# Optimization experiments

Hardware: AMD Instinct MI355X
Metric: run time of the kernel (lower is better)

The kernel has to match this reference:

```python
import jax, jax.numpy as jnp
import numpy as np

DIM = 512
NUM_HEADS = 8
DIM_HEAD = DIM // NUM_HEADS


def _xavier(key, shape):
    fan_in, fan_out = shape[0], shape[1]
    a = (6.0 / (fan_in + fan_out)) ** 0.5
    return jax.random.uniform(key, shape, jnp.float32, -a, a)


def setup_inputs() -> dict:
    key = jax.random.key(0)
    ks = jax.random.split(key, 8)
    B, N, M = 2, 2048, 2048
    x = jax.random.normal(ks[0], (B, N, DIM), jnp.float32)
    source = jax.random.normal(ks[1], (B, M, DIM), jnp.float32)
    source_mask = jax.random.randint(ks[2], (B, M), 0, 2) > 0
    Wq = _xavier(ks[3], (DIM, DIM)); bq = jnp.zeros((DIM,), jnp.float32)
    Wk = _xavier(ks[4], (DIM, DIM)); bk = jnp.zeros((DIM,), jnp.float32)
    Wv = _xavier(ks[5], (DIM, DIM)); bv = jnp.zeros((DIM,), jnp.float32)
    Wm = _xavier(ks[6], (DIM, DIM)); bm = jnp.zeros((DIM,), jnp.float32)
    return {"x": x, "source": source, "source_mask": source_mask,
            "Wq": Wq, "bq": bq, "Wk": Wk, "bk": bk,
            "Wv": Wv, "bv": bv, "Wm": Wm, "bm": bm}


def reference(x, source, source_mask, Wq, bq, Wk, bk, Wv, bv, Wm, bm):
    B, N, D = x.shape
    M = source.shape[-2]
    H, Dh = NUM_HEADS, DIM_HEAD
    # projections (torch Linear: x @ W^T + b)
    q = (x @ Wq.T + bq).reshape(B, N, H, Dh)
    k = (source @ Wk.T + bk).reshape(B, M, H, Dh)
    v = (source @ Wv.T + bv).reshape(B, M, H, Dh)
    scale = 1.0 / (Dh ** 0.5)
    # scores: [B, N, M, H]
    scores = jnp.einsum('bnhd,bmhd->bnmh', q, k) * scale
    scores = jnp.where(source_mask[:, None, :, None], scores, -jnp.inf)
    prob = jax.nn.softmax(scores, axis=-2)  # softmax over m
    agg = jnp.einsum('bnmh,bmhd->bnhd', prob, v).reshape(B, N, D)
    return agg @ Wm.T + bm
```

## Files before the change

### kernel.cpp

```cpp
#include <hip/hip_runtime.h>
#include <hip/hip_bf16.h>

#define DIMF 512
#define NHEAD 8
#define DHEAD 64
#define BATCH 2
#define SEQN 2048
#define SEQM 2048
#define FPS 40
#define QSCALE 0.18033688011112042f

typedef unsigned short u16;
typedef __attribute__((ext_vector_type(8))) short bf16x8;
typedef __attribute__((ext_vector_type(4))) float f32x4;

static __device__ __forceinline__ u16 f2bf(float f) {
    unsigned u = __float_as_uint(f);
    u += 0x7FFF + ((u >> 16) & 1);
    return (u16)(u >> 16);
}
static __device__ __forceinline__ u16 f2bf_fast(float f) {
    return (u16)((__float_as_uint(f) + 0x8000u) >> 16);
}

static __device__ __forceinline__
void load16(const u16* g, u16* l) {
    __builtin_amdgcn_global_load_lds(
        (const __attribute__((address_space(1))) void*)g,
        (__attribute__((address_space(3))) void*)l,
        16, 0, 0);
}

__global__ __launch_bounds__(256)
void cvt_w(const float* __restrict__ wq, const float* __restrict__ wk,
           const float* __restrict__ wv, const float* __restrict__ wm,
           const int* __restrict__ mask,
           u16* __restrict__ wqb, u16* __restrict__ wkb,
           u16* __restrict__ wvb, u16* __restrict__ wmb,
           u16* __restrict__ maskbf)
{
    int i = (blockIdx.x * 256 + threadIdx.x) * 4;
    if (blockIdx.y == 4) {
        if (i < BATCH * SEQM) {
            int4 m4 = *(const int4*)&mask[i];
            *(ushort4*)&maskbf[i] = make_ushort4(m4.x ? 0x3F80 : 0, m4.y ? 0x3F80 : 0,
                                                 m4.z ? 0x3F80 : 0, m4.w ? 0x3F80 : 0);
        }
        return;
    }
    const float* in = (blockIdx.y == 0) ? wq : (blockIdx.y == 1) ? wk
                    : (blockIdx.y == 2) ? wv : wm;
    u16* out = (blockIdx.y == 0) ? wqb : (blockIdx.y == 1) ? wkb
             : (blockIdx.y == 2) ? wvb : wmb;
    if (i >= DIMF * DIMF) return;
    float4 v = *(const float4*)&in[i];
    *(ushort4*)&out[i] = make_ushort4(f2bf(v.x), f2bf(v.y), f2bf(v.z), f2bf(v.w));
}

#define ASZ (64 * FPS)
#define BSZ (128 * FPS)

__device__ __forceinline__
void gemm_mfma(const float* __restrict__ Xf, const u16* __restrict__ Xb,
               const u16* __restrict__ W, const float* __restrict__ bias,
               const int* __restrict__ msk, void* __restrict__ Out, int mode)
{
    __shared__ __align__(16) u16 SH[2 * ASZ + 2 * BSZ];

    const int tid  = threadIdx.x;
    const int wave = tid >> 6;
    const int lane = tid & 63;
    const int l15  = lane & 15;
    const int quad = lane >> 4;
    const int wm = wave & 1, wn = wave >> 1;
    const int r0 = blockIdx.x * 64, c0 = blockIdx.y * 128;

    f32x4 acc[2][4] = {};

    const int br = tid >> 2, boct = tid & 3;
    const int ar = tid >> 3, aseg = tid & 7;

    bf16x8 rb0, rb1, rab;
    float4 ra0, ra1;

    auto loadg = [&](int k0) {
        rb0 = *(const bf16x8*)&W[(size_t)(c0 + br) * DIMF + k0 + boct * 8];
        rb1 = *(const bf16x8*)&W[(size_t)(c0 + br + 64) * DIMF + k0 + boct * 8];
        if (Xf) {
            ra0 = *(const float4*)&Xf[(size_t)(r0 + ar) * DIMF + k0 + aseg * 4];
            ra1 = *(const float4*)&Xf[(size_t)(r0 + ar + 32) * DIMF + k0 + aseg * 4];
        } else {
            rab = *(const bf16x8*)&Xb[(size_t)(r0 + br) * DIMF + k0 + boct * 8];
        }
    };
    auto stage = [&](int buf) {
        u16* As = SH + buf * ASZ;
        u16* Bs = SH + 2 * ASZ + buf * BSZ;
        if (Xf) {
            *(ushort4*)&As[ar * FPS + aseg * 4] =
                make_ushort4(f2bf(ra0.x), f2bf(ra0.y), f2bf(ra0.z), f2bf(ra0.w));
            *(ushort4*)&As[(ar + 32) * FPS + aseg * 4] =
                make_ushort4(f2bf(ra1.x), f2bf(ra1.y), f2bf(ra1.z), f2bf(ra1.w));
        } else {
            *(bf16x8*)&As[br * FPS + boct * 8] = rab;
        }
        *(bf16x8*)&Bs[br * FPS + boct * 8] = rb0;
        *(bf16x8*)&Bs[(br + 64) * FPS + boct * 8] = rb1;
    };

    loadg(0);
    stage(0);
    loadg(32);
    __syncthreads();

    const int NK = DIMF / 32;
    for (int kt = 0; kt < NK; ++kt) {
        const int cur = kt & 1;
        if (kt + 1 < NK) stage(cur ^ 1);
        if (kt + 2 < NK) loadg((kt + 2) * 32);
        const u16* As = SH + cur * ASZ;
        const u16* Bs = SH + 2 * ASZ + cur * BSZ;

        bf16x8 af[2], bf[4];
        #pragma unroll
        for (int mi = 0; mi < 2; ++mi)
            af[mi] = *(const bf16x8*)&As[(wm * 32 + mi * 16 + l15) * FPS + quad * 8];
        #pragma unroll
        for (int ni = 0; ni < 4; ++ni)
            bf[ni] = *(const bf16x8*)&Bs[(wn * 64 + ni * 16 + l15) * FPS + quad * 8];
        #pragma unroll
        for (int mi = 0; mi < 2; ++mi)
            #pragma unroll
            for (int ni = 0; ni < 4; ++ni)
                acc[mi][ni] = __builtin_amdgcn_mfma_f32_16x16x32_bf16(
                    af[mi], bf[ni], acc[mi][ni], 0, 0, 0);
        __syncthreads();
    }

    float bb[4];
    #pragma unroll
    for (int ni = 0; ni < 4; ++ni)
        bb[ni] = bias[c0 + wn * 64 + ni * 16 + l15];

    if (mode == 2) {
        u16* T = SH;
        const int b = r0 >> 11;
        const int n_base = r0 & (SEQN - 1);
        #pragma unroll
        for (int hh = 0; hh < 2; ++hh) {
            __syncthreads();
            if (wn == hh) {
                #pragma unroll
                for (int mi = 0; mi < 2; ++mi) {
                    const int rl = wm * 32 + mi * 16 + quad * 4;
                    int4 m4 = *(const int4*)&msk[b * SEQM + n_base + rl];
                    float mm[4];
                    mm[0] = m4.x ? 1.f : 0.f; mm[1] = m4.y ? 1.f : 0.f;
                    mm[2] = m4.z ? 1.f : 0.f; mm[3] = m4.w ? 1.f : 0.f;
                    #pragma unroll
                    for (int ni = 0; ni < 4; ++ni)
                        #pragma unroll
                        for (int r = 0; r < 4; ++r)
                            T[(rl + r) * 72 + ni * 16 + l15] =
                                f2bf((acc[mi][ni][r] + bb[ni]) * mm[r]);
                }
            }
            __syncthreads();
            const int d = tid >> 2, ms = (tid & 3) << 4;
            u16 tmp[16];
            #pragma unroll
            for (int j = 0; j < 16; ++j) tmp[j] = T[(ms + j) * 72 + d];
            const int hgl = (c0 >> 6) + hh;
            u16* dst = (u16*)Out + ((size_t)(b * NHEAD + hgl) * DHEAD + d) * SEQM
                       + n_base + ms;
            *(bf16x8*)&dst[0] = *(bf16x8*)&tmp[0];
            *(bf16x8*)&dst[8] = *(bf16x8*)&tmp[8];
        }
        return;
    }

    #pragma unroll
    for (int mi = 0; mi < 2; ++mi) {
        const int Rbase = r0 + wm * 32 + mi * 16 + quad * 4;
        const int b = Rbase >> 11;
        const int nb = Rbase & (SEQN - 1);
        #pragma unroll
        for (int ni = 0; ni < 4; ++ni) {
            const int C = c0 + wn * 64 + ni * 16 + l15;
            const int h = C >> 6, d = C & 63;
            if (mode == 0) {
                u16* ow = (u16*)Out;
                #pragma unroll
                for (int r = 0; r < 4; ++r)
                    ow[(((size_t)(b * NHEAD + h) * SEQN) + nb + r) * DHEAD + d] =
                        f2bf((acc[mi][ni][r] + bb[ni]) * QSCALE);
            } else if (mode == 1) {
                u16* ow = (u16*)Out;
                #pragma unroll
                for (int r = 0; r < 4; ++r)
                    ow[(((size_t)(b * NHEAD + h) * SEQN) + nb + r) * DHEAD + d] =
                        f2bf(acc[mi][ni][r] + bb[ni]);
            } else {
                float* ow = (float*)Out;
                #pragma unroll
                for (int r = 0; r < 4; ++r)
                    ow[(size_t)(Rbase + r) * DIMF + C] = acc[mi][ni][r] + bb[ni];
            }
        }
    }
}

__global__ __launch_bounds__(256, 3)
void qkv_proj(const float* __restrict__ x, const float* __restrict__ src,
              const u16* __restrict__ wqb, const float* __restrict__ bq,
              const u16* __restrict__ wkb, const float* __restrict__ bk,
              const u16* __restrict__ wvb, const float* __restrict__ bv,
              const int* __restrict__ mask,
              u16* __restrict__ qw, u16* __restrict__ kw, u16* __restrict__ vtw)
{
    const int z = blockIdx.z;
    const float* X = (z == 0) ? x : src;
    const u16* W = (z == 0) ? wqb : (z == 1) ? wkb : wvb;
    const float* B = (z == 0) ? bq : (z == 1) ? bk : bv;
    void* O = (z == 0) ? (void*)qw : (z == 1) ? (void*)kw : (void*)vtw;
    gemm_mfma(X, nullptr, W, B, mask, O, z);
}

__global__ __launch_bounds__(256, 3)
void out_proj(const u16* __restrict__ aggb, const u16* __restrict__ wmb,
              const float* __restrict__ bm, float* __restrict__ out)
{
    gemm_mfma(nullptr, aggb, wmb, bm, nullptr, (void*)out, 3);
}

__global__ __launch_bounds__(256, 2)
void flash_attn_mfma(const u16* __restrict__ q, const u16* __restrict__ k,
                     const u16* __restrict__ vt, const u16* __restrict__ maskbf,
                     u16* __restrict__ agg)
{
    __shared__ __align__(16) u16 KsD[2][4096];
    __shared__ __align__(16) u16 VtsD[2][4096];
    __shared__ u16 Ps[4 * 32 * FPS];
    float* Osum = (float*)&KsD[0][0];
    float* Lsum = (float*)&VtsD[0][0];

    const int tid  = threadIdx.x;
    const int wave = tid >> 6;
    const int lane = tid & 63;
    const int l15  = lane & 15;
    const int quad = lane >> 4;
    const int qg = wave >> 1, mh = wave & 1;

    const int bid  = blockIdx.x;
    const int xcd  = bid & 7, slot = bid >> 3;
    const int pair = (xcd << 1) | (slot & 1);
    const int b = pair >> 3, h = pair & 7;
    const int n0 = (slot >> 1) * 64;

    const size_t hoff = (size_t)(b * NHEAD + h) * (size_t)SEQM * DHEAD;
    const u16* kb = k  + hoff;
    const u16* vb = vt + hoff;
    const u16* mb = maskbf + b * SEQM;

    const int dr   = lane >> 3;
    const int doct = (lane & 7) ^ (dr & 7);
    const int g0 = wave, g1 = 4 + wave;
    const u16* kq0 = kb + (size_t)(g0 * 8 + dr) * DHEAD + doct * 8;
    const u16* kq1 = kb + (size_t)(g1 * 8 + dr) * DHEAD + doct * 8;
    const u16* vq0 = vb + (size_t)(g0 * 8 + dr) * SEQM + doct * 8;
    const u16* vq1 = vb + (size_t)(g1 * 8 + dr) * SEQM + doct * 8;

    bf16x8 qf[2][2];
    #pragma unroll
    for (int qh = 0; qh < 2; ++qh) {
        const u16* qp = q + hoff + (size_t)(n0 + qg * 32 + qh * 16 + l15) * DHEAD
                        + quad * 8;
        qf[qh][0] = *(const bf16x8*)qp;
        qf[qh][1] = *(const bf16x8*)(qp + 32);
    }

    load16(kq0, &KsD[0][g0 * 512]);
    load16(kq1, &KsD[0][g1 * 512]);
    load16(vq0, &VtsD[0][g0 * 512]);
    load16(vq1, &VtsD[0][g1 * 512]);
    bf16x8 mf_nxt = *(const bf16x8*)&mb[32 * mh + quad * 8];

    f32x4 O[2][4] = {};
    f32x4 lacc[2] = {};
    u16* Pw = Ps + wave * (32 * FPS);
    const int xoct = l15 & 7;

    for (int mt = 0; mt < SEQM / 64; ++mt) {
        const int cur = mt & 1;
        __syncthreads();
        bf16x8 mf = mf_nxt;
        if (mt + 1 < SEQM / 64) {
            const int m1 = (mt + 1) * 64;
            const int nb = cur ^ 1;
            load16(kq0 + (size_t)m1 * DHEAD, &KsD[nb][g0 * 512]);
            load16(kq1 + (size_t)m1 * DHEAD, &KsD[nb][g1 * 512]);
            load16(vq0 + m1, &VtsD[nb][g0 * 512]);
            load16(vq1 + m1, &VtsD[nb][g1 * 512]);
            mf_nxt = *(const bf16x8*)&mb[m1 + 32 * mh + quad * 8];
        }
        const u16* Ks  = KsD[cur];
        const u16* Vts = VtsD[cur];

        f32x4 st[2][2] = {};
        #pragma unroll
        for (int sub = 0; sub < 2; ++sub) {
            const int mrow = 32 * mh + 16 * sub + l15;
            #pragma unroll
            for (int c = 0; c < 2; ++c) {
                const int oct = (4 * c + quad) ^ xoct;
                bf16x8 af = *(const bf16x8*)&Ks[mrow * 64 + oct * 8];
                #pragma unroll
                for (int qh = 0; qh < 2; ++qh)
                    st[qh][sub] = __builtin_amdgcn_mfma_f32_16x16x32_bf16(
                        af, qf[qh][c], st[qh][sub], 0, 0, 0);
            }
        }

        #pragma unroll
        for (int qh = 0; qh < 2; ++qh)
            #pragma unroll
            for (int sub = 0; sub < 2; ++sub) {
                ushort4 w4 = make_ushort4(
                    f2bf_fast(__builtin_amdgcn_exp2f(st[qh][sub][0])),
                    f2bf_fast(__builtin_amdgcn_exp2f(st[qh][sub][1])),
                    f2bf_fast(__builtin_amdgcn_exp2f(st[qh][sub][2])),
                    f2bf_fast(__builtin_amdgcn_exp2f(st[qh][sub][3])));
                *(ushort4*)&Pw[(qh * 16 + l15) * FPS + 16 * sub + 4 * quad] = w4;
            }

        bf16x8 vf[4];
        #pragma unroll
        for (int sd = 0; sd < 4; ++sd) {
            const int oct = (4 * mh + quad) ^ xoct;
            vf[sd] = *(const bf16x8*)&Vts[(16 * sd + l15) * 64 + oct * 8];
        }

        #pragma unroll
        for (int qh = 0; qh < 2; ++qh) {
            bf16x8 pf = *(const bf16x8*)&Pw[(qh * 16 + l15) * FPS + quad * 8];
            lacc[qh] = __builtin_amdgcn_mfma_f32_16x16x32_bf16(pf, mf, lacc[qh], 0, 0, 0);
            #pragma unroll
            for (int sd = 0; sd < 4; ++sd)
                O[qh][sd] = __builtin_amdgcn_mfma_f32_16x16x32_bf16(
                    pf, vf[sd], O[qh][sd], 0, 0, 0);
        }
    }

    __syncthreads();
    if (mh == 1) {
        #pragma unroll
        for (int qh = 0; qh < 2; ++qh) {
            #pragma unroll
            for (int sd = 0; sd < 4; ++sd)
                #pragma unroll
                for (int r = 0; r < 4; ++r)
                    Osum[qg * 2048 + (qh * 16 + quad * 4 + r) * 64 + 16 * sd + l15]
                        = O[qh][sd][r];
            if (l15 == 0) {
                #pragma unroll
                for (int r = 0; r < 4; ++r)
                    Lsum[qg * 32 + qh * 16 + quad * 4 + r] = lacc[qh][r];
            }
        }
    }
    __syncthreads();
    if (mh == 0) {
        #pragma unroll
        for (int qh = 0; qh < 2; ++qh)
            #pragma unroll
            for (int r = 0; r < 4; ++r) {
                const float inv = 1.f /
                    (lacc[qh][r] + Lsum[qg * 32 + qh * 16 + quad * 4 + r]);
                const int n = n0 + qg * 32 + qh * 16 + quad * 4 + r;
                u16* ag = agg + ((size_t)b * SEQN + n) * DIMF + h * DHEAD + l15;
                #pragma unroll
                for (int sd = 0; sd < 4; ++sd)
                    ag[16 * sd] = f2bf((O[qh][sd][r] +
                        Osum[qg * 2048 + (qh * 16 + quad * 4 + r) * 64 + 16 * sd + l15])
                        * inv);
            }
    }
}

extern "C" void kernel_launch(void* const* d_in, const int* in_sizes, int n_in,
                              void* d_out, int out_size, void* d_ws, size_t ws_size,
                              hipStream_t stream)
{
    (void)in_sizes; (void)n_in; (void)out_size; (void)ws_size;
    const float* x      = (const float*)d_in[0];
    const float* source = (const float*)d_in[1];
    const int*   mask   = (const int*)  d_in[2];
    const float* Wq = (const float*)d_in[3]; const float* bq = (const float*)d_in[4];
    const float* Wk = (const float*)d_in[5]; const float* bk = (const float*)d_in[6];
    const float* Wv = (const float*)d_in[7]; const float* bv = (const float*)d_in[8];
    const float* Wm = (const float*)d_in[9]; const float* bm = (const float*)d_in[10];
    float* out = (float*)d_out;

    const size_t SZ = (size_t)BATCH * SEQN * DIMF;
    const size_t WZ = (size_t)DIMF * DIMF;
    u16* qw   = (u16*)d_ws;
    u16* kw   = qw  + SZ;
    u16* vtw  = kw  + SZ;
    u16* aggb = vtw + SZ;
    u16* wqb  = aggb + SZ;
    u16* wkb  = wqb + WZ;
    u16* wvb  = wkb + WZ;
    u16* wmb  = wvb + WZ;
    u16* maskbf = wmb + WZ;

    dim3 gcvt((WZ / 4 + 255) / 256, 5);
    cvt_w<<<gcvt, 256, 0, stream>>>(Wq, Wk, Wv, Wm, mask,
                                    wqb, wkb, wvb, wmb, maskbf);

    dim3 gproj(4096 / 64, 512 / 128, 3);
    qkv_proj<<<gproj, 256, 0, stream>>>(x, source, wqb, bq, wkb, bk, wvb, bv,
                                        mask, qw, kw, vtw);

    flash_attn_mfma<<<512, 256, 0, stream>>>(qw, kw, vtw, maskbf, aggb);

    dim3 gout(4096 / 64, 512 / 128);
    out_proj<<<gout, 256, 0, stream>>>(aggb, wmb, bm, out);
}
```

Measured before the change: 147.6 us.

## Fuse weight/mask conversion into consumers and halve attention query tile

New measurement: 158.8 us. +7.5%, slower.

```diff
diff --git a/kernel.cpp b/kernel.cpp
--- a/kernel.cpp
+++ b/kernel.cpp
@@ -22,6 +22,19 @@
 static __device__ __forceinline__ u16 f2bf_fast(float f) {
     return (u16)((__float_as_uint(f) + 0x8000u) >> 16);
 }
+static __device__ __forceinline__ ushort4 cvt4(float4 v) {
+    return make_ushort4(f2bf(v.x), f2bf(v.y), f2bf(v.z), f2bf(v.w));
+}
+static __device__ __forceinline__ bf16x8 mask8(const int* p) {
+    int4 a = *(const int4*)p;
+    int4 b = *(const int4*)(p + 4);
+    union { u16 u[8]; bf16x8 v; } r;
+    r.u[0] = a.x ? 0x3F80 : 0; r.u[1] = a.y ? 0x3F80 : 0;
+    r.u[2] = a.z ? 0x3F80 : 0; r.u[3] = a.w ? 0x3F80 : 0;
+    r.u[4] = b.x ? 0x3F80 : 0; r.u[5] = b.y ? 0x3F80 : 0;
+    r.u[6] = b.z ? 0x3F80 : 0; r.u[7] = b.w ? 0x3F80 : 0;
+    return r.v;
+}
 
 static __device__ __forceinline__
 void load16(const u16* g, u16* l) {
@@ -31,38 +44,12 @@
         16, 0, 0);
 }
 
-__global__ __launch_bounds__(256)
-void cvt_w(const float* __restrict__ wq, const float* __restrict__ wk,
-           const float* __restrict__ wv, const float* __restrict__ wm,
-           const int* __restrict__ mask,
-           u16* __restrict__ wqb, u16* __restrict__ wkb,
-           u16* __restrict__ wvb, u16* __restrict__ wmb,
-           u16* __restrict__ maskbf)
-{
-    int i = (blockIdx.x * 256 + threadIdx.x) * 4;
-    if (blockIdx.y == 4) {
-        if (i < BATCH * SEQM) {
-            int4 m4 = *(const int4*)&mask[i];
-            *(ushort4*)&maskbf[i] = make_ushort4(m4.x ? 0x3F80 : 0, m4.y ? 0x3F80 : 0,
-                                                 m4.z ? 0x3F80 : 0, m4.w ? 0x3F80 : 0);
-        }
-        return;
-    }
-    const float* in = (blockIdx.y == 0) ? wq : (blockIdx.y == 1) ? wk
-                    : (blockIdx.y == 2) ? wv : wm;
-    u16* out = (blockIdx.y == 0) ? wqb : (blockIdx.y == 1) ? wkb
-             : (blockIdx.y == 2) ? wvb : wmb;
-    if (i >= DIMF * DIMF) return;
-    float4 v = *(const float4*)&in[i];
-    *(ushort4*)&out[i] = make_ushort4(f2bf(v.x), f2bf(v.y), f2bf(v.z), f2bf(v.w));
-}
-
 #define ASZ (64 * FPS)
 #define BSZ (128 * FPS)
 
 __device__ __forceinline__
 void gemm_mfma(const float* __restrict__ Xf, const u16* __restrict__ Xb,
-               const u16* __restrict__ W, const float* __restrict__ bias,
+               const float* __restrict__ Wf, const float* __restrict__ bias,
                const int* __restrict__ msk, void* __restrict__ Out, int mode)
 {
     __shared__ __align__(16) u16 SH[2 * ASZ + 2 * BSZ];
@@ -77,15 +64,18 @@
 
     f32x4 acc[2][4] = {};
 
+    const int wr = tid >> 1, wh = (tid & 1) * 16;
+    const int ar = tid >> 3, aseg = tid & 7;
     const int br = tid >> 2, boct = tid & 3;
-    const int ar = tid >> 3, aseg = tid & 7;
-
-    bf16x8 rb0, rb1, rab;
+
+    float4 rw[4];
     float4 ra0, ra1;
+    bf16x8 rab;
 
     auto loadg = [&](int k0) {
-        rb0 = *(const bf16x8*)&W[(size_t)(c0 + br) * DIMF + k0 + boct * 8];
-        rb1 = *(const bf16x8*)&W[(size_t)(c0 + br + 64) * DIMF + k0 + boct * 8];
+        #pragma unroll
+        for (int j = 0; j < 4; ++j)
+            rw[j] = *(const float4*)&Wf[(size_t)(c0 + wr) * DIMF + k0 + wh + 4 * j];
         if (Xf) {
             ra0 = *(const float4*)&Xf[(size_t)(r0 + ar) * DIMF + k0 + aseg * 4];
             ra1 = *(const float4*)&Xf[(size_t)(r0 + ar + 32) * DIMF + k0 + aseg * 4];
@@ -97,15 +87,14 @@
         u16* As = SH + buf * ASZ;
         u16* Bs = SH + 2 * ASZ + buf * BSZ;
         if (Xf) {
-            *(ushort4*)&As[ar * FPS + aseg * 4] =
-                make_ushort4(f2bf(ra0.x), f2bf(ra0.y), f2bf(ra0.z), f2bf(ra0.w));
-            *(ushort4*)&As[(ar + 32) * FPS + aseg * 4] =
-                make_ushort4(f2bf(ra1.x), f2bf(ra1.y), f2bf(ra1.z), f2bf(ra1.w));
+            *(ushort4*)&As[ar * FPS + aseg * 4] = cvt4(ra0);
+            *(ushort4*)&As[(ar + 32) * FPS + aseg * 4] = cvt4(ra1);
         } else {
             *(bf16x8*)&As[br * FPS + boct * 8] = rab;
         }
-        *(bf16x8*)&Bs[br * FPS + boct * 8] = rb0;
-        *(bf16x8*)&Bs[(br + 64) * FPS + boct * 8] = rb1;
+        #pragma unroll
+        for (int j = 0; j < 4; ++j)
+            *(ushort4*)&Bs[wr * FPS + wh + 4 * j] = cvt4(rw[j]);
     };
 
     loadg(0);
@@ -212,35 +201,35 @@
 
 __global__ __launch_bounds__(256, 3)
 void qkv_proj(const float* __restrict__ x, const float* __restrict__ src,
-              const u16* __restrict__ wqb, const float* __restrict__ bq,
-              const u16* __restrict__ wkb, const float* __restrict__ bk,
-              const u16* __restrict__ wvb, const float* __restrict__ bv,
+              const float* __restrict__ Wq, const float* __restrict__ bq,
+              const float* __restrict__ Wk, const float* __restrict__ bk,
+              const float* __restrict__ Wv, const float* __restrict__ bv,
               const int* __restrict__ mask,
               u16* __restrict__ qw, u16* __restrict__ kw, u16* __restrict__ vtw)
 {
     const int z = blockIdx.z;
     const float* X = (z == 0) ? x : src;
-    const u16* W = (z == 0) ? wqb : (z == 1) ? wkb : wvb;
+    const float* W = (z == 0) ? Wq : (z == 1) ? Wk : Wv;
     const float* B = (z == 0) ? bq : (z == 1) ? bk : bv;
     void* O = (z == 0) ? (void*)qw : (z == 1) ? (void*)kw : (void*)vtw;
     gemm_mfma(X, nullptr, W, B, mask, O, z);
 }
 
 __global__ __launch_bounds__(256, 3)
-void out_proj(const u16* __restrict__ aggb, const u16* __restrict__ wmb,
+void out_proj(const u16* __restrict__ aggb, const float* __restrict__ Wm,
               const float* __restrict__ bm, float* __restrict__ out)
 {
-    gemm_mfma(nullptr, aggb, wmb, bm, nullptr, (void*)out, 3);
-}
-
-__global__ __launch_bounds__(256, 2)
+    gemm_mfma(nullptr, aggb, Wm, bm, nullptr, (void*)out, 3);
+}
+
+__global__ __launch_bounds__(256, 4)
 void flash_attn_mfma(const u16* __restrict__ q, const u16* __restrict__ k,
-                     const u16* __restrict__ vt, const u16* __restrict__ maskbf,
+                     const u16* __restrict__ vt, const int* __restrict__ mask,
                      u16* __restrict__ agg)
 {
     __shared__ __align__(16) u16 KsD[2][4096];
     __shared__ __align__(16) u16 VtsD[2][4096];
-    __shared__ u16 Ps[4 * 32 * FPS];
+    __shared__ u16 Ps[4 * 16 * FPS];
     float* Osum = (float*)&KsD[0][0];
     float* Lsum = (float*)&VtsD[0][0];
 
@@ -255,12 +244,12 @@
     const int xcd  = bid & 7, slot = bid >> 3;
     const int pair = (xcd << 1) | (slot & 1);
     const int b = pair >> 3, h = pair & 7;
-    const int n0 = (slot >> 1) * 64;
+    const int n0 = (slot >> 1) * 32;
 
     const size_t hoff = (size_t)(b * NHEAD + h) * (size_t)SEQM * DHEAD;
     const u16* kb = k  + hoff;
     const u16* vb = vt + hoff;
-    const u16* mb = maskbf + b * SEQM;
+    const int* mg = mask + b * SEQM;
 
     const int dr   = lane >> 3;
     const int doct = (lane & 7) ^ (dr & 7);
@@ -270,24 +259,22 @@
     const u16* vq0 = vb + (size_t)(g0 * 8 + dr) * SEQM + doct * 8;
     const u16* vq1 = vb + (size_t)(g1 * 8 + dr) * SEQM + doct * 8;
 
-    bf16x8 qf[2][2];
-    #pragma unroll
-    for (int qh = 0; qh < 2; ++qh) {
-        const u16* qp = q + hoff + (size_t)(n0 + qg * 32 + qh * 16 + l15) * DHEAD
-                        + quad * 8;
-        qf[qh][0] = *(const bf16x8*)qp;
-        qf[qh][1] = *(const bf16x8*)(qp + 32);
+    bf16x8 qf[2];
+    {
+        const u16* qp = q + hoff + (size_t)(n0 + qg * 16 + l15) * DHEAD + quad * 8;
+        qf[0] = *(const bf16x8*)qp;
+        qf[1] = *(const bf16x8*)(qp + 32);
     }
 
     load16(kq0, &KsD[0][g0 * 512]);
     load16(kq1, &KsD[0][g1 * 512]);
     load16(vq0, &VtsD[0][g0 * 512]);
     load16(vq1, &VtsD[0][g1 * 512]);
-    bf16x8 mf_nxt = *(const bf16x8*)&mb[32 * mh + quad * 8];
-
-    f32x4 O[2][4] = {};
-    f32x4 lacc[2] = {};
-    u16* Pw = Ps + wave * (32 * FPS);
+    bf16x8 mf_nxt = mask8(&mg[32 * mh + quad * 8]);
+
+    f32x4 O[4] = {};
+    f32x4 lacc = {};
+    u16* Pw = Ps + wave * (16 * FPS);
     const int xoct = l15 & 7;
 
     for (int mt = 0; mt < SEQM / 64; ++mt) {
@@ -301,12 +288,12 @@
             load16(kq1 + (size_t)m1 * DHEAD, &KsD[nb][g1 * 512]);
             load16(vq0 + m1, &VtsD[nb][g0 * 512]);
             load16(vq1 + m1, &VtsD[nb][g1 * 512]);
-            mf_nxt = *(const bf16x8*)&mb[m1 + 32 * mh + quad * 8];
+            mf_nxt = mask8(&mg[m1 + 32 * mh + quad * 8]);
         }
         const u16* Ks  = KsD[cur];
         const u16* Vts = VtsD[cur];
 
-        f32x4 st[2][2] = {};
+        f32x4 st[2] = {};
         #pragma unroll
         for (int sub = 0; sub < 2; ++sub) {
             const int mrow = 32 * mh + 16 * sub + l15;
@@ -314,76 +301,55 @@
             for (int c = 0; c < 2; ++c) {
                 const int oct = (4 * c + quad) ^ xoct;
                 bf16x8 af = *(const bf16x8*)&Ks[mrow * 64 + oct * 8];
-                #pragma unroll
-                for (int qh = 0; qh < 2; ++qh)
-                    st[qh][sub] = __builtin_amdgcn_mfma_f32_16x16x32_bf16(
-                        af, qf[qh][c], st[qh][sub], 0, 0, 0);
+                st[sub] = __builtin_amdgcn_mfma_f32_16x16x32_bf16(
+                    af, qf[c], st[sub], 0, 0, 0);
             }
         }
 
         #pragma unroll
-        for (int qh = 0; qh < 2; ++qh)
-            #pragma unroll
-            for (int sub = 0; sub < 2; ++sub) {
-                ushort4 w4 = make_ushort4(
-                    f2bf_fast(__builtin_amdgcn_exp2f(st[qh][sub][0])),
-                    f2bf_fast(__builtin_amdgcn_exp2f(st[qh][sub][1])),
-                    f2bf_fast(__builtin_amdgcn_exp2f(st[qh][sub][2])),
-                    f2bf_fast(__builtin_amdgcn_exp2f(st[qh][sub][3])));
-                *(ushort4*)&Pw[(qh * 16 + l15) * FPS + 16 * sub + 4 * quad] = w4;
-            }
-
-        bf16x8 vf[4];
+        for (int sub = 0; sub < 2; ++sub) {
+            ushort4 w4 = make_ushort4(
+                f2bf_fast(__builtin_amdgcn_exp2f(st[sub][0])),
+                f2bf_fast(__builtin_amdgcn_exp2f(st[sub][1])),
+                f2bf_fast(__builtin_amdgcn_exp2f(st[sub][2])),
+                f2bf_fast(__builtin_amdgcn_exp2f(st[sub][3])));
+            *(ushort4*)&Pw[l15 * FPS + 16 * sub + 4 * quad] = w4;
+        }
+
+        bf16x8 pf = *(const bf16x8*)&Pw[l15 * FPS + quad * 8];
+        lacc = __builtin_amdgcn_mfma_f32_16x16x32_bf16(pf, mf, lacc, 0, 0, 0);
         #pragma unroll
         for (int sd = 0; sd < 4; ++sd) {
             const int oct = (4 * mh + quad) ^ xoct;
-            vf[sd] = *(const bf16x8*)&Vts[(16 * sd + l15) * 64 + oct * 8];
-        }
-
-        #pragma unroll
-        for (int qh = 0; qh < 2; ++qh) {
-            bf16x8 pf = *(const bf16x8*)&Pw[(qh * 16 + l15) * FPS + quad * 8];
-            lacc[qh] = __builtin_amdgcn_mfma_f32_16x16x32_bf16(pf, mf, lacc[qh], 0, 0, 0);
-            #pragma unroll
-            for (int sd = 0; sd < 4; ++sd)
-                O[qh][sd] = __builtin_amdgcn_mfma_f32_16x16x32_bf16(
-                    pf, vf[sd], O[qh][sd], 0, 0, 0);
+            bf16x8 vf = *(const bf16x8*)&Vts[(16 * sd + l15) * 64 + oct * 8];
+            O[sd] = __builtin_amdgcn_mfma_f32_16x16x32_bf16(pf, vf, O[sd], 0, 0, 0);
         }
     }
 
     __syncthreads();
     if (mh == 1) {
         #pragma unroll
-        for (int qh = 0; qh < 2; ++qh) {
-            #pragma unroll
-            for (int sd = 0; sd < 4; ++sd)
-                #pragma unroll
-                for (int r = 0; r < 4; ++r)
-                    Osum[qg * 2048 + (qh * 16 + quad * 4 + r) * 64 + 16 * sd + l15]
-                        = O[qh][sd][r];
-            if (l15 == 0) {
-                #pragma unroll
-                for (int r = 0; r < 4; ++r)
-                    Lsum[qg * 32 + qh * 16 + quad * 4 + r] = lacc[qh][r];
-            }
+        for (int sd = 0; sd < 4; ++sd)
+            #pragma unroll
+            for (int r = 0; r < 4; ++r)
+                Osum[qg * 1024 + (quad * 4 + r) * 64 + 16 * sd + l15] = O[sd][r];
+        if (l15 == 0) {
+            #pragma unroll
+            for (int r = 0; r < 4; ++r) Lsum[qg * 16 + quad * 4 + r] = lacc[r];
         }
     }
     __syncthreads();
     if (mh == 0) {
         #pragma unroll
-        for (int qh = 0; qh < 2; ++qh)
-            #pragma unroll
-            for (int r = 0; r < 4; ++r) {
-                const float inv = 1.f /
-                    (lacc[qh][r] + Lsum[qg * 32 + qh * 16 + quad * 4 + r]);
-                const int n = n0 + qg * 32 + qh * 16 + quad * 4 + r;
-                u16* ag = agg + ((size_t)b * SEQN + n) * DIMF + h * DHEAD + l15;
-                #pragma unroll
-                for (int sd = 0; sd < 4; ++sd)
-                    ag[16 * sd] = f2bf((O[qh][sd][r] +
-                        Osum[qg * 2048 + (qh * 16 + quad * 4 + r) * 64 + 16 * sd + l15])
-                        * inv);
-            }
+        for (int r = 0; r < 4; ++r) {
+            const float inv = 1.f / (lacc[r] + Lsum[qg * 16 + quad * 4 + r]);
+            const int n = n0 + qg * 16 + quad * 4 + r;
+            u16* ag = agg + ((size_t)b * SEQN + n) * DIMF + h * DHEAD + l15;
+            #pragma unroll
+            for (int sd = 0; sd < 4; ++sd)
+                ag[16 * sd] = f2bf((O[sd][r] +
+                    Osum[qg * 1024 + (quad * 4 + r) * 64 + 16 * sd + l15]) * inv);
+        }
     }
 }
 
@@ -402,27 +368,17 @@
     float* out = (float*)d_out;
 
     const size_t SZ = (size_t)BATCH * SEQN * DIMF;
-    const size_t WZ = (size_t)DIMF * DIMF;
     u16* qw   = (u16*)d_ws;
     u16* kw   = qw  + SZ;
     u16* vtw  = kw  + SZ;
     u16* aggb = vtw + SZ;
-    u16* wqb  = aggb + SZ;
-    u16* wkb  = wqb + WZ;
-    u16* wvb  = wkb + WZ;
-    u16* wmb  = wvb + WZ;
-    u16* maskbf = wmb + WZ;
-
-    dim3 gcvt((WZ / 4 + 255) / 256, 5);
-    cvt_w<<<gcvt, 256, 0, stream>>>(Wq, Wk, Wv, Wm, mask,
-                                    wqb, wkb, wvb, wmb, maskbf);
 
     dim3 gproj(4096 / 64, 512 / 128, 3);
-    qkv_proj<<<gproj, 256, 0, stream>>>(x, source, wqb, bq, wkb, bk, wvb, bv,
+    qkv_proj<<<gproj, 256, 0, stream>>>(x, source, Wq, bq, Wk, bk, Wv, bv,
                                         mask, qw, kw, vtw);
 
-    flash_attn_mfma<<<512, 256, 0, stream>>>(qw, kw, vtw, maskbf, aggb);
+    flash_attn_mfma<<<1024, 256, 0, stream>>>(qw, kw, vtw, mask, aggb);
 
     dim3 gout(4096 / 64, 512 / 128);
-    out_proj<<<gout, 256, 0, stream>>>(aggb, wmb, bm, out);
-}
+    out_proj<<<gout, 256, 0, stream>>>(aggb, Wm, bm, out);
+}
```
